# Optimization experiments

Hardware: AMD Instinct MI355X
Metric: run time of the kernel (lower is better)

The kernel has to match this reference:

```python
import jax, jax.numpy as jnp
import numpy as np

B, S, H = 2, 2048, 1024
NUM_HEADS = 16


def setup_inputs() -> dict:
    key = jax.random.key(0)
    ks = jax.random.split(key, 5)
    scale = 1.0 / np.sqrt(H)
    x = jax.random.normal(ks[0], (B, S, H), dtype=jnp.float32)
    W_qkv = jax.random.normal(ks[1], (3 * H, H), dtype=jnp.float32) * scale
    b_qkv = jax.random.normal(ks[2], (3 * H,), dtype=jnp.float32) * 0.02
    W_o = jax.random.normal(ks[3], (H, H), dtype=jnp.float32) * scale
    b_o = jax.random.normal(ks[4], (H,), dtype=jnp.float32) * 0.02
    return {"x": x, "W_qkv": W_qkv, "b_qkv": b_qkv, "W_o": W_o, "b_o": b_o}


def reference(x, W_qkv, b_qkv, W_o, b_o):
    b, s, h = x.shape
    n = NUM_HEADS
    d_head = h // n
    # QKV projection (torch Linear: x @ W.T + b), then chunk into Q, K, V
    qkv = x @ W_qkv.T + b_qkv                      # [b, s, 3h]
    Q, K, V = jnp.split(qkv, 3, axis=-1)           # each [b, s, h]
    # split heads: b s (n d) -> b n s d
    Q = Q.reshape(b, s, n, d_head).transpose(0, 2, 1, 3)
    K = K.reshape(b, s, n, d_head).transpose(0, 2, 1, 3)
    V = V.reshape(b, s, n, d_head).transpose(0, 2, 1, 3)
    # scores, causal mask, scale (mask before/after scale is equivalent: -inf stays -inf)
    scores = jnp.einsum('bnqd,bnkd->bnqk', Q, K) / jnp.sqrt(jnp.float32(d_head))
    causal = jnp.tril(jnp.ones((s, s), dtype=bool))  # True = keep
    scores = jnp.where(causal, scores, -jnp.inf)
    A = jax.nn.softmax(scores, axis=-1)
    AV = jnp.einsum('bnqk,bnkd->bnqd', A, V)
    out = AV.transpose(0, 2, 1, 3).reshape(b, s, h)  # merge heads
    return out @ W_o.T + b_o
```

## Files before the change

### kernel.cpp

```cpp
#include <hip/hip_runtime.h>
#include <cstdint>
#include <cstddef>

#define BATCH 2
#define SEQ   2048
#define HID   1024
#define NHEAD 16
#define DHEAD 64
#define QKV_N 3072
#define NTOK  4096

typedef __attribute__((ext_vector_type(4))) float f32x4;
typedef __attribute__((ext_vector_type(8))) short bf16x8;

#define QSCL 0.18033688011112042f

__device__ inline unsigned short f2bf(float f) {
    union { float f; unsigned int u; } v; v.f = f;
    unsigned int u = v.u;
    unsigned int r = (u + 0x7fffu + ((u >> 16) & 1u)) >> 16;
    return (unsigned short)r;
}

__device__ __forceinline__ void gload_lds16(const void* g, void* l) {
    __builtin_amdgcn_global_load_lds(
        (const __attribute__((address_space(1))) void*)g,
        (__attribute__((address_space(3))) void*)l, 16, 0, 0);
}

__global__ void cast_f32_bf16(const float* __restrict__ in, unsigned short* __restrict__ out, int n4) {
    int i = blockIdx.x * blockDim.x + threadIdx.x;
    if (i >= n4) return;
    float4 v = reinterpret_cast<const float4*>(in)[i];
    ushort4 o;
    o.x = f2bf(v.x); o.y = f2bf(v.y); o.z = f2bf(v.z); o.w = f2bf(v.w);
    reinterpret_cast<ushort4*>(out)[i] = o;
}

template<int BN, int OUT_MODE>
__global__ __launch_bounds__(256) void gemm_bt(const short* __restrict__ A,
                                               const short* __restrict__ B,
                                               const float* __restrict__ bias,
                                               void* __restrict__ Cout,
                                               int M, int N, int K) {
    constexpr int WTN = BN / 2;
    constexpr int NJ  = WTN / 16;
    constexpr int NBC = BN / 64;

    __shared__ short sA[2][128 * 32];
    __shared__ short sB[2][BN * 32];

    const int tid  = threadIdx.x;
    const int lane = tid & 63;
    const int wave = tid >> 6;
    const int wm = wave >> 1, wn = wave & 1;

    const int nwg = gridDim.x;
    const int swz = (blockIdx.x & 7) * (nwg >> 3) + (blockIdx.x >> 3);
    const int tiles_n = N / BN;
    const int m0 = (swz / tiles_n) * 128;
    const int n0 = (swz % tiles_n) * BN;

    f32x4 acc[4][NJ];
    #pragma unroll
    for (int i = 0; i < 4; ++i)
        #pragma unroll
        for (int j = 0; j < NJ; ++j) acc[i][j] = (f32x4){0.f, 0.f, 0.f, 0.f};

    const int r = lane & 15;
    const int G = lane >> 4;

    #define GSTAGE(kt_, buf_)                                                          \
        {                                                                              \
            _Pragma("unroll")                                                          \
            for (int i = 0; i < 2; ++i) {                                              \
                int ga = (i * 4 + wave) * 64 + lane;                                   \
                int row = ga >> 2, gcol = (ga & 3) ^ (row & 3);                        \
                gload_lds16(A + (size_t)(m0 + row) * K + (kt_) + gcol * 8,             \
                            &sA[buf_][(i * 4 + wave) * 512]);                          \
            }                                                                          \
            _Pragma("unroll")                                                          \
            for (int i = 0; i < NBC; ++i) {                                            \
                int gb = (i * 4 + wave) * 64 + lane;                                   \
                int row = gb >> 2, gcol = (gb & 3) ^ (row & 3);                        \
                gload_lds16(B + (size_t)(n0 + row) * K + (kt_) + gcol * 8,             \
                            &sB[buf_][(i * 4 + wave) * 512]);                          \
            }                                                                          \
        }

    GSTAGE(0, 0);
    __syncthreads();
    int cur = 0;

    const int nsteps = K >> 5;
    for (int ks = 0; ks < nsteps; ++ks) {
        if (ks + 1 < nsteps) GSTAGE((ks + 1) * 32, cur ^ 1);

        const int sg = G ^ (r & 3);
        bf16x8 af[4], bfr[NJ];
        #pragma unroll
        for (int i = 0; i < 4; ++i) {
            int row = wm * 64 + i * 16 + r;
            af[i] = *reinterpret_cast<const bf16x8*>(&sA[cur][row * 32 + sg * 8]);
        }
        #pragma unroll
        for (int j = 0; j < NJ; ++j) {
            int row = wn * WTN + j * 16 + r;
            bfr[j] = *reinterpret_cast<const bf16x8*>(&sB[cur][row * 32 + sg * 8]);
        }
        #pragma unroll
        for (int i = 0; i < 4; ++i)
            #pragma unroll
            for (int j = 0; j < NJ; ++j)
                acc[i][j] = __builtin_amdgcn_mfma_f32_16x16x32_bf16(af[i], bfr[j], acc[i][j], 0, 0, 0);

        __syncthreads();
        cur ^= 1;
    }
    #undef GSTAGE

    const int col_l = lane & 15;
    const int row_g = (lane >> 4) * 4;
    #pragma unroll
    for (int i = 0; i < 4; ++i) {
        #pragma unroll
        for (int j = 0; j < NJ; ++j) {
            int nn = n0 + wn * WTN + j * 16 + col_l;
            float bv = bias[nn];
            float scl = (OUT_MODE == 2 && nn < HID) ? QSCL : 1.0f;
            #pragma unroll
            for (int reg = 0; reg < 4; ++reg) {
                int mm = m0 + wm * 64 + i * 16 + row_g + reg;
                float v = (acc[i][j][reg] + bv) * scl;
                if (OUT_MODE == 0) {
                    reinterpret_cast<float*>(Cout)[(size_t)mm * N + nn] = v;
                } else {
                    reinterpret_cast<unsigned short*>(Cout)[(size_t)mm * N + nn] = f2bf(v);
                }
            }
        }
    }
}

#define TLDP 72
__global__ __launch_bounds__(256) void transpose_v(const short* __restrict__ qkv,
                                                   short* __restrict__ vP) {
    const int st = blockIdx.x;
    const int bh = blockIdx.y;
    const int b  = bh >> 4, h = bh & 15;
    __shared__ short ld[64 * TLDP];
    const int tid = threadIdx.x;

    #pragma unroll
    for (int i = 0; i < 2; ++i) {
        int idx = i * 256 + tid;
        int row = idx >> 3, c = idx & 7;
        int4 v = *reinterpret_cast<const int4*>(
            qkv + ((size_t)(b * SEQ + st * 64 + row)) * QKV_N + 2 * HID + h * DHEAD + c * 8);
        *reinterpret_cast<int4*>(&ld[row * TLDP + c * 8]) = v;
    }
    __syncthreads();
    #pragma unroll
    for (int i = 0; i < 2; ++i) {
        int u  = i * 256 + tid;
        int Tp = u >> 8;
        int d  = (u >> 2) & 63;
        int p  = u & 3;
        int b0 = Tp * 32 + 4 * p;
        int b1 = b0 + 16;
        ushort4 o0, o1;
        o0.x = (unsigned short)ld[(b0 + 0) * TLDP + d];
        o0.y = (unsigned short)ld[(b0 + 1) * TLDP + d];
        o0.z = (unsigned short)ld[(b0 + 2) * TLDP + d];
        o0.w = (unsigned short)ld[(b0 + 3) * TLDP + d];
        o1.x = (unsigned short)ld[(b1 + 0) * TLDP + d];
        o1.y = (unsigned short)ld[(b1 + 1) * TLDP + d];
        o1.z = (unsigned short)ld[(b1 + 2) * TLDP + d];
        o1.w = (unsigned short)ld[(b1 + 3) * TLDP + d];
        size_t out = ((size_t)((bh * 64 + st * 2 + Tp) * 64 + d)) * 32 + p * 8;
        *reinterpret_cast<ushort4*>(&vP[out])     = o0;
        *reinterpret_cast<ushort4*>(&vP[out + 4]) = o1;
    }
}

__global__ __launch_bounds__(128) void attn_fwd(const short* __restrict__ qkv,
                                                const short* __restrict__ vP,
                                                short* __restrict__ av) {
    const int bid = blockIdx.x;
    const int qb  = 63 - (bid >> 5);
    const int bh  = bid & 31;
    const int b   = bh >> 4;
    const int h   = bh & 15;

    __shared__ float comb[32][68];

    const int tid  = threadIdx.x;
    const int lane = tid & 63;
    const int wave = tid >> 6;
    const int r    = lane & 15;
    const int G    = lane >> 4;
    const int row_g = G * 4;

    const int qbw = qb * 32;

    bf16x8 qf[2][2];
    #pragma unroll
    for (int mi = 0; mi < 2; ++mi) {
        const short* Qg = qkv + ((size_t)(b * SEQ + qbw + mi * 16 + r)) * QKV_N + h * DHEAD;
        qf[mi][0] = *reinterpret_cast<const bf16x8*>(Qg + G * 8);
        qf[mi][1] = *reinterpret_cast<const bf16x8*>(Qg + 32 + G * 8);
    }

    f32x4 oacc[2][4];
    f32x4 oL[2];
    #pragma unroll
    for (int mi = 0; mi < 2; ++mi) {
        oL[mi] = (f32x4){0.f, 0.f, 0.f, 0.f};
        #pragma unroll
        for (int dg = 0; dg < 4; ++dg) oacc[mi][dg] = (f32x4){0.f, 0.f, 0.f, 0.f};
    }

    bf16x8 ones;
    #pragma unroll
    for (int e = 0; e < 8; ++e) ones[e] = (short)0x3f80;

    const short* kp0 = qkv + (size_t)(b * SEQ) * QKV_N + HID + h * DHEAD;
    const short* vp0 = vP + (size_t)(bh * 64) * 2048;
    const int koff0 = r * QKV_N + G * 8;
    const int koff1 = (16 + r) * QKV_N + G * 8;
    const int voffb = r * 32 + G * 8;

    for (int t = wave; t <= qb; t += 2) {
        const short* kpt = kp0 + (size_t)t * 32 * QKV_N;
        const short* vpt = vp0 + (size_t)t * 2048;

        int4 k00 = *reinterpret_cast<const int4*>(kpt + koff0);
        int4 k01 = *reinterpret_cast<const int4*>(kpt + koff0 + 32);
        int4 k10 = *reinterpret_cast<const int4*>(kpt + koff1);
        int4 k11 = *reinterpret_cast<const int4*>(kpt + koff1 + 32);
        int4 v0 = *reinterpret_cast<const int4*>(vpt + voffb);
        int4 v1 = *reinterpret_cast<const int4*>(vpt + voffb + 16 * 32);
        int4 v2 = *reinterpret_cast<const int4*>(vpt + voffb + 32 * 32);
        int4 v3 = *reinterpret_cast<const int4*>(vpt + voffb + 48 * 32);

        bf16x8 kb[2][2], vb[4];
        __builtin_memcpy(&kb[0][0], &k00, 16);
        __builtin_memcpy(&kb[0][1], &k01, 16);
        __builtin_memcpy(&kb[1][0], &k10, 16);
        __builtin_memcpy(&kb[1][1], &k11, 16);
        __builtin_memcpy(&vb[0], &v0, 16);
        __builtin_memcpy(&vb[1], &v1, 16);
        __builtin_memcpy(&vb[2], &v2, 16);
        __builtin_memcpy(&vb[3], &v3, 16);

        const bool diag = (t == qb);

        #pragma unroll
        for (int mi = 0; mi < 2; ++mi) {
            f32x4 s[2];
            #pragma unroll
            for (int g = 0; g < 2; ++g) {
                f32x4 z = (f32x4){0.f, 0.f, 0.f, 0.f};
                z = __builtin_amdgcn_mfma_f32_16x16x32_bf16(kb[g][0], qf[mi][0], z, 0, 0, 0);
                z = __builtin_amdgcn_mfma_f32_16x16x32_bf16(kb[g][1], qf[mi][1], z, 0, 0, 0);
                s[g] = z;
            }
            if (diag) {
                int ql = mi * 16 + r;
                #pragma unroll
                for (int g = 0; g < 2; ++g) {
                    #pragma unroll
                    for (int reg = 0; reg < 4; ++reg) {
                        int kvl = g * 16 + row_g + reg;
                        if (kvl > ql) s[g][reg] = -30000.f;
                    }
                }
            }
            unsigned int w0, w1, w2, w3;
            {
                float p0 = __builtin_amdgcn_exp2f(s[0][0]);
                float p1 = __builtin_amdgcn_exp2f(s[0][1]);
                float p2 = __builtin_amdgcn_exp2f(s[0][2]);
                float p3 = __builtin_amdgcn_exp2f(s[0][3]);
                float p4 = __builtin_amdgcn_exp2f(s[1][0]);
                float p5 = __builtin_amdgcn_exp2f(s[1][1]);
                float p6 = __builtin_amdgcn_exp2f(s[1][2]);
                float p7 = __builtin_amdgcn_exp2f(s[1][3]);
                w0 = (unsigned int)f2bf(p0) | ((unsigned int)f2bf(p1) << 16);
                w1 = (unsigned int)f2bf(p2) | ((unsigned int)f2bf(p3) << 16);
                w2 = (unsigned int)f2bf(p4) | ((unsigned int)f2bf(p5) << 16);
                w3 = (unsigned int)f2bf(p6) | ((unsigned int)f2bf(p7) << 16);
            }
            bf16x8 pb;
            { int4 f; f.x = (int)w0; f.y = (int)w1; f.z = (int)w2; f.w = (int)w3;
              __builtin_memcpy(&pb, &f, 16); }

            #pragma unroll
            for (int dg = 0; dg < 4; ++dg)
                oacc[mi][dg] = __builtin_amdgcn_mfma_f32_16x16x32_bf16(vb[dg], pb, oacc[mi][dg], 0, 0, 0);
            oL[mi] = __builtin_amdgcn_mfma_f32_16x16x32_bf16(ones, pb, oL[mi], 0, 0, 0);
        }
    }

    if (wave == 0) {
        #pragma unroll
        for (int mi = 0; mi < 2; ++mi) {
            #pragma unroll
            for (int dg = 0; dg < 4; ++dg)
                *reinterpret_cast<f32x4*>(&comb[mi * 16 + r][dg * 16 + row_g]) = oacc[mi][dg];
            if (G == 0) comb[mi * 16 + r][64] = oL[mi][0];
        }
    }
    __syncthreads();
    if (wave == 1) {
        #pragma unroll
        for (int mi = 0; mi < 2; ++mi) {
            float l = comb[mi * 16 + r][64] + oL[mi][0];
            float il = 1.0f / l;
            size_t tok = (size_t)(b * SEQ + qbw + mi * 16 + r);
            #pragma unroll
            for (int dg = 0; dg < 4; ++dg) {
                f32x4 tot = *reinterpret_cast<f32x4*>(&comb[mi * 16 + r][dg * 16 + row_g]);
                tot = tot + oacc[mi][dg];
                ushort4 o;
                o.x = f2bf(tot[0] * il);
                o.y = f2bf(tot[1] * il);
                o.z = f2bf(tot[2] * il);
                o.w = f2bf(tot[3] * il);
                *reinterpret_cast<ushort4*>(&av[tok * HID + h * DHEAD + dg * 16 + row_g]) = o;
            }
        }
    }
}

extern "C" void kernel_launch(void* const* d_in, const int* in_sizes, int n_in,
                              void* d_out, int out_size, void* d_ws, size_t ws_size,
                              hipStream_t stream) {
    const float* x     = (const float*)d_in[0];
    const float* W_qkv = (const float*)d_in[1];
    const float* b_qkv = (const float*)d_in[2];
    const float* W_o   = (const float*)d_in[3];
    const float* b_o   = (const float*)d_in[4];
    float* out = (float*)d_out;

    const int n_x    = NTOK * HID;
    const int n_wqkv = QKV_N * HID;
    const int n_wo   = HID * HID;
    const int n_qkv  = NTOK * QKV_N;
    const int n_av   = NTOK * HID;

    short* xb    = (short*)d_ws;
    short* wqkvb = xb + n_x;
    short* wob   = wqkvb + n_wqkv;
    short* qkv   = wob + n_wo;
    short* av    = qkv + n_qkv;
    short* vP    = av + n_av;

    cast_f32_bf16<<<n_x / 1024,    256, 0, stream>>>(x,     (unsigned short*)xb,    n_x / 4);
    cast_f32_bf16<<<n_wqkv / 1024, 256, 0, stream>>>(W_qkv, (unsigned short*)wqkvb, n_wqkv / 4);
    cast_f32_bf16<<<n_wo / 1024,   256, 0, stream>>>(W_o,   (unsigned short*)wob,   n_wo / 4);

    gemm_bt<128, 2><<<(NTOK / 128) * (QKV_N / 128), 256, 0, stream>>>(
        xb, wqkvb, b_qkv, (void*)qkv, NTOK, QKV_N, HID);

    transpose_v<<<dim3(SEQ / 64, BATCH * NHEAD), 256, 0, stream>>>(qkv, vP);

    attn_fwd<<<2048, 128, 0, stream>>>(qkv, vP, av);

    gemm_bt<64, 0><<<(NTOK / 128) * (HID / 64), 256, 0, stream>>>(
        av, wob, b_o, (void*)out, NTOK, HID, HID);
}
```

Measured before the change: 128.5 us.

## Enlarge attention query tile to 64 rows with four waves splitting KV

The attention kernel now handles 64 query rows per block with 256 threads (4 waves), each wave striding over KV tiles by 4, and the grid is halved to 1024 blocks. Each K/V tile loaded into registers is reused across four 16-row query sub-tiles instead of two, which halves K/V global traffic per query. The causal mask now covers the two diagonal KV tiles using global indices. The cost is a serial three-stage reduction through LDS with extra barriers, more accumulator registers per thread (lower occupancy), and fewer blocks for load balancing.

```diff
diff --git a/kernel.cpp b/kernel.cpp
--- a/kernel.cpp
+++ b/kernel.cpp
@@ -183,16 +183,16 @@
     }
 }
 
-__global__ __launch_bounds__(128) void attn_fwd(const short* __restrict__ qkv,
+__global__ __launch_bounds__(256) void attn_fwd(const short* __restrict__ qkv,
                                                 const short* __restrict__ vP,
                                                 short* __restrict__ av) {
     const int bid = blockIdx.x;
-    const int qb  = 63 - (bid >> 5);
+    const int qb  = 31 - (bid >> 5);
     const int bh  = bid & 31;
     const int b   = bh >> 4;
     const int h   = bh & 15;
 
-    __shared__ float comb[32][68];
+    __shared__ float comb[64][68];
 
     const int tid  = threadIdx.x;
     const int lane = tid & 63;
@@ -201,20 +201,20 @@
     const int G    = lane >> 4;
     const int row_g = G * 4;
 
-    const int qbw = qb * 32;
-
-    bf16x8 qf[2][2];
-    #pragma unroll
-    for (int mi = 0; mi < 2; ++mi) {
+    const int qbw = qb * 64;
+
+    bf16x8 qf[4][2];
+    #pragma unroll
+    for (int mi = 0; mi < 4; ++mi) {
         const short* Qg = qkv + ((size_t)(b * SEQ + qbw + mi * 16 + r)) * QKV_N + h * DHEAD;
         qf[mi][0] = *reinterpret_cast<const bf16x8*>(Qg + G * 8);
         qf[mi][1] = *reinterpret_cast<const bf16x8*>(Qg + 32 + G * 8);
     }
 
-    f32x4 oacc[2][4];
-    f32x4 oL[2];
-    #pragma unroll
-    for (int mi = 0; mi < 2; ++mi) {
+    f32x4 oacc[4][4];
+    f32x4 oL[4];
+    #pragma unroll
+    for (int mi = 0; mi < 4; ++mi) {
         oL[mi] = (f32x4){0.f, 0.f, 0.f, 0.f};
         #pragma unroll
         for (int dg = 0; dg < 4; ++dg) oacc[mi][dg] = (f32x4){0.f, 0.f, 0.f, 0.f};
@@ -230,7 +230,8 @@
     const int koff1 = (16 + r) * QKV_N + G * 8;
     const int voffb = r * 32 + G * 8;
 
-    for (int t = wave; t <= qb; t += 2) {
+    const int tlast = 2 * qb + 1;
+    for (int t = wave; t <= tlast; t += 4) {
         const short* kpt = kp0 + (size_t)t * 32 * QKV_N;
         const short* vpt = vp0 + (size_t)t * 2048;
 
@@ -253,10 +254,10 @@
         __builtin_memcpy(&vb[2], &v2, 16);
         __builtin_memcpy(&vb[3], &v3, 16);
 
-        const bool diag = (t == qb);
-
-        #pragma unroll
-        for (int mi = 0; mi < 2; ++mi) {
+        const bool band = (t >= 2 * qb);
+
+        #pragma unroll
+        for (int mi = 0; mi < 4; ++mi) {
             f32x4 s[2];
             #pragma unroll
             for (int g = 0; g < 2; ++g) {
@@ -265,14 +266,14 @@
                 z = __builtin_amdgcn_mfma_f32_16x16x32_bf16(kb[g][1], qf[mi][1], z, 0, 0, 0);
                 s[g] = z;
             }
-            if (diag) {
-                int ql = mi * 16 + r;
+            if (band) {
+                int qg = qbw + mi * 16 + r;
                 #pragma unroll
                 for (int g = 0; g < 2; ++g) {
                     #pragma unroll
                     for (int reg = 0; reg < 4; ++reg) {
-                        int kvl = g * 16 + row_g + reg;
-                        if (kvl > ql) s[g][reg] = -30000.f;
+                        int kvg = t * 32 + g * 16 + row_g + reg;
+                        if (kvg > qg) s[g][reg] = -30000.f;
                     }
                 }
             }
@@ -302,9 +303,10 @@
         }
     }
 
+    __syncthreads();
     if (wave == 0) {
         #pragma unroll
-        for (int mi = 0; mi < 2; ++mi) {
+        for (int mi = 0; mi < 4; ++mi) {
             #pragma unroll
             for (int dg = 0; dg < 4; ++dg)
                 *reinterpret_cast<f32x4*>(&comb[mi * 16 + r][dg * 16 + row_g]) = oacc[mi][dg];
@@ -314,7 +316,31 @@
     __syncthreads();
     if (wave == 1) {
         #pragma unroll
-        for (int mi = 0; mi < 2; ++mi) {
+        for (int mi = 0; mi < 4; ++mi) {
+            #pragma unroll
+            for (int dg = 0; dg < 4; ++dg) {
+                f32x4 c = *reinterpret_cast<f32x4*>(&comb[mi * 16 + r][dg * 16 + row_g]);
+                *reinterpret_cast<f32x4*>(&comb[mi * 16 + r][dg * 16 + row_g]) = c + oacc[mi][dg];
+            }
+            if (G == 0) comb[mi * 16 + r][64] += oL[mi][0];
+        }
+    }
+    __syncthreads();
+    if (wave == 2) {
+        #pragma unroll
+        for (int mi = 0; mi < 4; ++mi) {
+            #pragma unroll
+            for (int dg = 0; dg < 4; ++dg) {
+                f32x4 c = *reinterpret_cast<f32x4*>(&comb[mi * 16 + r][dg * 16 + row_g]);
+                *reinterpret_cast<f32x4*>(&comb[mi * 16 + r][dg * 16 + row_g]) = c + oacc[mi][dg];
+            }
+            if (G == 0) comb[mi * 16 + r][64] += oL[mi][0];
+        }
+    }
+    __syncthreads();
+    if (wave == 3) {
+        #pragma unroll
+        for (int mi = 0; mi < 4; ++mi) {
             float l = comb[mi * 16 + r][64] + oL[mi][0];
             float il = 1.0f / l;
             size_t tok = (size_t)(b * SEQ + qbw + mi * 16 + r);
@@ -365,7 +391,7 @@
 
     transpose_v<<<dim3(SEQ / 64, BATCH * NHEAD), 256, 0, stream>>>(qkv, vP);
 
-    attn_fwd<<<2048, 128, 0, stream>>>(qkv, vP, av);
+    attn_fwd<<<1024, 256, 0, stream>>>(qkv, vP, av);
 
     gemm_bt<64, 0><<<(NTOK / 128) * (HID / 64), 256, 0, stream>>>(
         av, wob, b_o, (void*)out, NTOK, HID, HID);
```

Measured after the change: 115.5 us. 1.11x faster.
